# Performance work log

Hardware: AMD Instinct MI355X
Metric: run time of the kernel (lower is better)

Reference implementation:

```python
import jax, jax.numpy as jnp
import numpy as np

EPS_NORM = 1e-12
EPS_POS = 1e-05
MARGIN = 0.5


def l2_norm(x):
    # matches torch: x / sqrt(sum(x^2, axis=1) + 1e-12)
    norm = jnp.sqrt(jnp.sum(x * x, axis=1) + EPS_NORM)
    return x / norm[:, None]


def setup_inputs() -> dict:
    key = jax.random.key(0)
    k1, k2, k3, k4 = jax.random.split(key, 4)
    n, d, n_classes = 8192, 1024, 1024
    inputs_col = jax.random.normal(k1, (n, d), dtype=jnp.float32)
    inputs_row = jax.random.normal(k2, (n, d), dtype=jnp.float32)
    targets_col = jax.random.randint(k3, (n,), 0, n_classes)
    target_row = jax.random.randint(k4, (n,), 0, n_classes)
    return {"inputs_col": inputs_col, "targets_col": targets_col,
            "inputs_row": inputs_row, "target_row": target_row}


def reference(inputs_col, targets_col, inputs_row, target_row):
    n = inputs_col.shape[0]
    # [n, n] cosine similarity matrix
    sim = l2_norm(inputs_col) @ l2_norm(inputs_row).T
    same = targets_col[:, None] == target_row[None, :]  # [n, n] bool
    pos_mask = same & (sim < 1.0 - EPS_POS)
    neg_mask = (~same) & (sim > MARGIN)
    pos_loss = jnp.sum(jnp.where(pos_mask, 1.0 - sim, 0.0), axis=1)  # [n]
    neg_loss = jnp.sum(jnp.where(neg_mask, sim, 0.0), axis=1)        # [n]
    has_pos = jnp.any(pos_mask, axis=1)  # rows without valid positives are skipped
    row_loss = jnp.where(has_pos, pos_loss + neg_loss, 0.0)
    return jnp.sum(row_loss) / n
```

## Files before the change

kernel.cpp:

```cpp
#include <hip/hip_runtime.h>


constexpr int N = 8192;
constexpr int D = 1024;
constexpr int NT = D / 32;

typedef short bf16x8 __attribute__((ext_vector_type(8)));
typedef float f32x4 __attribute__((ext_vector_type(4)));

static __device__ inline unsigned short f2bf(float f) {
  unsigned int u = __float_as_uint(f);
  unsigned int r = (u + 0x7fffu + ((u >> 16) & 1u)) >> 16;
  return (unsigned short)r;
}

__global__ __launch_bounds__(256) void normalize_kernel(
    const float* __restrict__ in_col, const float* __restrict__ in_row,
    unsigned short* __restrict__ out_col, unsigned short* __restrict__ out_row,
    unsigned int* __restrict__ zeroBase) {
  if (blockIdx.x < 96) zeroBase[blockIdx.x * 256 + threadIdx.x] = 0u;

  int r = blockIdx.x * 4 + (threadIdx.x >> 6);
  int lane = threadIdx.x & 63;
  const float* in =
      (r < N) ? in_col + (size_t)r * D : in_row + (size_t)(r - N) * D;
  unsigned short* out =
      (r < N) ? out_col + (size_t)r * D : out_row + (size_t)(r - N) * D;
  float4 v[4];
  float s = 0.f;
#pragma unroll
  for (int c = 0; c < 4; c++) {
    v[c] = ((const float4*)in)[lane + c * 64];
    s += v[c].x * v[c].x + v[c].y * v[c].y + v[c].z * v[c].z + v[c].w * v[c].w;
  }
#pragma unroll
  for (int off = 32; off >= 1; off >>= 1) s += __shfl_xor(s, off, 64);
  float inv = 1.0f / sqrtf(s + 1e-12f);
#pragma unroll
  for (int c = 0; c < 4; c++) {
    ushort4 o;
    o.x = f2bf(v[c].x * inv);
    o.y = f2bf(v[c].y * inv);
    o.z = f2bf(v[c].z * inv);
    o.w = f2bf(v[c].w * inv);
    ((ushort4*)out)[lane + c * 64] = o;
  }
}

__global__ __launch_bounds__(256, 2) void loss_kernel(
    const unsigned short* __restrict__ An, const unsigned short* __restrict__ Bn,
    const int* __restrict__ tc, const int* __restrict__ tr,
    float* __restrict__ lossG, int* __restrict__ hasG) {
  __shared__ unsigned short lds[24576];
  char* ldsb = (char*)lds;
  const char* ldsc = (const char*)lds;

  const int tid = threadIdx.x;
  const int lane = tid & 63;
  const int wid = tid >> 6;
  const int wr = wid >> 1;
  const int wc = wid & 1;

  const int bid = blockIdx.x;
  const int xcd = bid & 7, s = bid >> 3;
  const int iBase = (s >> 3) * 256;
  const int jBase = (xcd * 8 + (s & 7)) * 128;

  const int frow = lane & 15;
  const int kx = ((lane >> 4) * 16) ^ ((lane & 6) << 3);
  int rowA[8], rowB[4];
#pragma unroll
  for (int m = 0; m < 8; m++) rowA[m] = (wr * 128 + m * 16 + frow) * 64;
#pragma unroll
  for (int n = 0; n < 4; n++) rowB[n] = 32768 + (wc * 64 + n * 16 + frow) * 64;

  const int srow = tid >> 2;
  const int c16 = tid & 3;
  const int kswz = (c16 ^ ((srow >> 1) & 3)) * 8;
  const unsigned short* aS[4];
  const unsigned short* bS[2];
#pragma unroll
  for (int p = 0; p < 4; p++)
    aS[p] = An + (size_t)(iBase + srow + 64 * p) * D + kswz;
#pragma unroll
  for (int p = 0; p < 2; p++)
    bS[p] = Bn + (size_t)(jBase + srow + 64 * p) * D + kswz;

#define GLDS(g, l)                                                        \
  __builtin_amdgcn_global_load_lds(                                       \
      (const __attribute__((address_space(1))) void*)(g),                 \
      (__attribute__((address_space(3))) void*)(l), 16, 0, 0)

#define STAGE(tt, P)                                                          \
  do {                                                                        \
    const int _ko = ((tt) & 31) * 32;                                         \
    _Pragma("unroll") for (int p = 0; p < 4; p++)                             \
        GLDS(aS[p] + _ko, ldsb + (P)*16384 + p * 4096 + wid * 1024);          \
    _Pragma("unroll") for (int p = 0; p < 2; p++)                             \
        GLDS(bS[p] + _ko, ldsb + 32768 + (P)*8192 + p * 4096 + wid * 1024);   \
  } while (0)

  f32x4 acc[8][4];
#pragma unroll
  for (int mi = 0; mi < 8; mi++)
#pragma unroll
    for (int ni = 0; ni < 4; ni++) acc[mi][ni] = (f32x4){0.f, 0.f, 0.f, 0.f};

  bf16x8 af[8], bf[4];

  STAGE(0, 0);
  __syncthreads();

#define TILE(T, P)                                                            \
  do {                                                                        \
    STAGE((T) + 1, 1 - (P));                                                  \
    _Pragma("unroll") for (int m = 0; m < 8; m++)                             \
        af[m] = *(const bf16x8*)(ldsc + (P)*16384 + rowA[m] + kx);            \
    _Pragma("unroll") for (int n = 0; n < 4; n++)                             \
        bf[n] = *(const bf16x8*)(ldsc + (P)*8192 + rowB[n] + kx);             \
    _Pragma("unroll") for (int m = 0; m < 8; m++)                             \
        _Pragma("unroll") for (int n = 0; n < 4; n++)                         \
            acc[m][n] = __builtin_amdgcn_mfma_f32_16x16x32_bf16(              \
                af[m], bf[n], acc[m][n], 0, 0, 0);                            \
    __syncthreads();                                                          \
  } while (0)

  for (int t2 = 0; t2 < NT / 2; ++t2) {
    const int t0 = 2 * t2;
    TILE(t0, 0);
    TILE(t0 + 1, 1);
  }
#undef TILE
#undef STAGE
#undef GLDS

  int trj[4];
#pragma unroll
  for (int ni = 0; ni < 4; ni++) trj[ni] = tr[jBase + wc * 64 + ni * 16 + frow];

#pragma unroll
  for (int mi = 0; mi < 8; mi++) {
#pragma unroll
    for (int r = 0; r < 4; r++) {
      const int i = iBase + wr * 128 + mi * 16 + (lane >> 4) * 4 + r;
      const int tci = tc[i];
      float v = 0.f;
      bool hasp = false;
#pragma unroll
      for (int ni = 0; ni < 4; ni++) {
        float s2 = acc[mi][ni][r];
        if (tci == trj[ni]) {
          if (s2 < 1.0f - 1e-5f) { v += 1.0f - s2; hasp = true; }
        } else if (s2 > 0.5f) {
          v += s2;
        }
      }
#pragma unroll
      for (int off = 1; off < 16; off <<= 1) v += __shfl_xor(v, off, 16);
      unsigned long long m = __ballot(hasp);
      bool rowHas = ((m >> ((lane >> 4) * 16)) & 0xFFFFull) != 0;
      if ((lane & 15) == 0) {
        if (v != 0.f) atomicAdd(&lossG[i], v);
        if (rowHas) atomicOr(&hasG[i], 1);
      }
    }
  }
}

__global__ __launch_bounds__(1024) void finalize_kernel(
    const float* __restrict__ lossG, const int* __restrict__ hasG,
    float* __restrict__ out) {
  int tid = threadIdx.x;
  float s = 0.f;
  for (int i = tid; i < N; i += 1024)
    if (hasG[i]) s += lossG[i];
#pragma unroll
  for (int off = 32; off >= 1; off >>= 1) s += __shfl_xor(s, off, 64);
  __shared__ float w16[16];
  if ((tid & 63) == 0) w16[tid >> 6] = s;
  __syncthreads();
  if (tid == 0) {
    float t = 0.f;
#pragma unroll
    for (int w = 0; w < 16; w++) t += w16[w];
    out[0] = t / (float)N;
  }
}

extern "C" void kernel_launch(void* const* d_in, const int* in_sizes, int n_in,
                              void* d_out, int out_size, void* d_ws, size_t ws_size,
                              hipStream_t stream) {
  const float* in_col = (const float*)d_in[0];
  const int* tcol = (const int*)d_in[1];
  const float* in_row = (const float*)d_in[2];
  const int* trow = (const int*)d_in[3];
  float* out = (float*)d_out;

  char* ws = (char*)d_ws;
  float* lossG = (float*)ws;
  int* hasG = (int*)(ws + (size_t)N * 4);
  unsigned short* colN = (unsigned short*)(ws + (size_t)N * 8);
  unsigned short* rowN = colN + (size_t)N * D;

  normalize_kernel<<<(2 * N) / 4, 256, 0, stream>>>(in_col, in_row, colN, rowN,
                                                    (unsigned int*)ws);
  loss_kernel<<<2048, 256, 0, stream>>>(colN, rowN, tcol, trow, lossG, hasG);
  finalize_kernel<<<1, 1024, 0, stream>>>(lossG, hasG, out);
}
```

Baseline: 288.7 us.

## Switch similarity GEMM to FP8 e4m3 with scaled MFMA 16x16x128

The normalize kernel now writes the L2-normalized rows as FP8 e4m3 instead of bf16. The loss kernel uses the MI355X scaled f8f6f4 MFMA with K=128 per instruction, on 128x128 output tiles and a 4096-block grid, with a reworked LDS swizzle. This halves the operand bytes and raises matrix throughput per instruction. The risk is accuracy: FP8 rounding of the similarities can flip threshold comparisons near 0.5 and 1-1e-5, which changes the loss value.

```diff
diff --git a/kernel.cpp b/kernel.cpp
--- a/kernel.cpp
+++ b/kernel.cpp
@@ -3,29 +3,40 @@
 
 constexpr int N = 8192;
 constexpr int D = 1024;
-constexpr int NT = D / 32;
-
-typedef short bf16x8 __attribute__((ext_vector_type(8)));
+
+typedef int i32x4 __attribute__((ext_vector_type(4)));
+typedef int i32x8 __attribute__((ext_vector_type(8)));
 typedef float f32x4 __attribute__((ext_vector_type(4)));
 
-static __device__ inline unsigned short f2bf(float f) {
-  unsigned int u = __float_as_uint(f);
-  unsigned int r = (u + 0x7fffu + ((u >> 16) & 1u)) >> 16;
-  return (unsigned short)r;
+static __device__ inline unsigned int f2fp8(float x) {
+  unsigned int u = __float_as_uint(x);
+  unsigned int sgn = (u >> 24) & 0x80u;
+  float a = __uint_as_float(u & 0x7fffffffu);
+  unsigned int bits;
+  if (a < 0.015625f) {
+    bits = (unsigned int)__float2int_rn(a * 512.0f);
+  } else {
+    unsigned int v = __float_as_uint(a);
+    unsigned int e = v >> 23;
+    unsigned int m = v & 0x7fffffu;
+    unsigned int mr = (m + 0x7ffffu + ((m >> 20) & 1u)) >> 20;
+    bits = ((e - 120u) << 3) + mr;
+  }
+  return sgn | bits;
 }
 
 __global__ __launch_bounds__(256) void normalize_kernel(
     const float* __restrict__ in_col, const float* __restrict__ in_row,
-    unsigned short* __restrict__ out_col, unsigned short* __restrict__ out_row,
+    unsigned int* __restrict__ out_col, unsigned int* __restrict__ out_row,
     unsigned int* __restrict__ zeroBase) {
-  if (blockIdx.x < 96) zeroBase[blockIdx.x * 256 + threadIdx.x] = 0u;
+  if (blockIdx.x < 64) zeroBase[blockIdx.x * 256 + threadIdx.x] = 0u;
 
   int r = blockIdx.x * 4 + (threadIdx.x >> 6);
   int lane = threadIdx.x & 63;
   const float* in =
       (r < N) ? in_col + (size_t)r * D : in_row + (size_t)(r - N) * D;
-  unsigned short* out =
-      (r < N) ? out_col + (size_t)r * D : out_row + (size_t)(r - N) * D;
+  unsigned int* out =
+      ((r < N) ? out_col : out_row) + (size_t)(r < N ? r : r - N) * (D / 4);
   float4 v[4];
   float s = 0.f;
 #pragma unroll
@@ -38,22 +49,17 @@
   float inv = 1.0f / sqrtf(s + 1e-12f);
 #pragma unroll
   for (int c = 0; c < 4; c++) {
-    ushort4 o;
-    o.x = f2bf(v[c].x * inv);
-    o.y = f2bf(v[c].y * inv);
-    o.z = f2bf(v[c].z * inv);
-    o.w = f2bf(v[c].w * inv);
-    ((ushort4*)out)[lane + c * 64] = o;
+    unsigned int u = f2fp8(v[c].x * inv) | (f2fp8(v[c].y * inv) << 8) |
+                     (f2fp8(v[c].z * inv) << 16) | (f2fp8(v[c].w * inv) << 24);
+    out[lane + c * 64] = u;
   }
 }
 
 __global__ __launch_bounds__(256, 2) void loss_kernel(
-    const unsigned short* __restrict__ An, const unsigned short* __restrict__ Bn,
+    const unsigned char* __restrict__ An, const unsigned char* __restrict__ Bn,
     const int* __restrict__ tc, const int* __restrict__ tr,
     float* __restrict__ lossG, int* __restrict__ hasG) {
-  __shared__ unsigned short lds[24576];
-  char* ldsb = (char*)lds;
-  const char* ldsc = (const char*)lds;
+  __shared__ char lds[65536];
 
   const int tid = threadIdx.x;
   const int lane = tid & 63;
@@ -63,93 +69,100 @@
 
   const int bid = blockIdx.x;
   const int xcd = bid & 7, s = bid >> 3;
-  const int iBase = (s >> 3) * 256;
+  const int iBase = (s >> 3) * 128;
   const int jBase = (xcd * 8 + (s & 7)) * 128;
 
   const int frow = lane & 15;
-  const int kx = ((lane >> 4) * 16) ^ ((lane & 6) << 3);
-  int rowA[8], rowB[4];
-#pragma unroll
-  for (int m = 0; m < 8; m++) rowA[m] = (wr * 128 + m * 16 + frow) * 64;
-#pragma unroll
-  for (int n = 0; n < 4; n++) rowB[n] = 32768 + (wc * 64 + n * 16 + frow) * 64;
-
-  const int srow = tid >> 2;
-  const int c16 = tid & 3;
-  const int kswz = (c16 ^ ((srow >> 1) & 3)) * 8;
-  const unsigned short* aS[4];
-  const unsigned short* bS[2];
-#pragma unroll
-  for (int p = 0; p < 4; p++)
-    aS[p] = An + (size_t)(iBase + srow + 64 * p) * D + kswz;
-#pragma unroll
-  for (int p = 0; p < 2; p++)
-    bS[p] = Bn + (size_t)(jBase + srow + 64 * p) * D + kswz;
+  const int cg = lane >> 4;
+  const int klo = ((2 * cg) ^ (frow & 7)) * 16;
+  const int khi = ((2 * cg + 1) ^ (frow & 7)) * 16;
+  int rowA[4], rowB[4];
+#pragma unroll
+  for (int f = 0; f < 4; f++) rowA[f] = (wr * 64 + f * 16 + frow) * 128;
+#pragma unroll
+  for (int f = 0; f < 4; f++)
+    rowB[f] = 32768 + (wc * 64 + f * 16 + frow) * 128;
+
+  const int srow = tid >> 3;
+  const int schunk = (tid & 7) ^ ((tid >> 3) & 7);
+  const unsigned char* aS[4];
+  const unsigned char* bS[4];
+#pragma unroll
+  for (int i = 0; i < 4; i++) {
+    aS[i] = An + (size_t)(iBase + i * 32 + srow) * D + schunk * 16;
+    bS[i] = Bn + (size_t)(jBase + i * 32 + srow) * D + schunk * 16;
+  }
 
 #define GLDS(g, l)                                                        \
   __builtin_amdgcn_global_load_lds(                                       \
       (const __attribute__((address_space(1))) void*)(g),                 \
       (__attribute__((address_space(3))) void*)(l), 16, 0, 0)
 
-#define STAGE(tt, P)                                                          \
-  do {                                                                        \
-    const int _ko = ((tt) & 31) * 32;                                         \
-    _Pragma("unroll") for (int p = 0; p < 4; p++)                             \
-        GLDS(aS[p] + _ko, ldsb + (P)*16384 + p * 4096 + wid * 1024);          \
-    _Pragma("unroll") for (int p = 0; p < 2; p++)                             \
-        GLDS(bS[p] + _ko, ldsb + 32768 + (P)*8192 + p * 4096 + wid * 1024);   \
+#define STAGE(st, P)                                                      \
+  do {                                                                    \
+    _Pragma("unroll") for (int i = 0; i < 4; i++)                         \
+        GLDS(aS[i] + (st) * 128, lds + (P)*16384 + i * 4096 + wid * 1024);\
+    _Pragma("unroll") for (int i = 0; i < 4; i++)                         \
+        GLDS(bS[i] + (st) * 128,                                          \
+             lds + 32768 + (P)*16384 + i * 4096 + wid * 1024);            \
   } while (0)
 
-  f32x4 acc[8][4];
-#pragma unroll
-  for (int mi = 0; mi < 8; mi++)
-#pragma unroll
-    for (int ni = 0; ni < 4; ni++) acc[mi][ni] = (f32x4){0.f, 0.f, 0.f, 0.f};
-
-  bf16x8 af[8], bf[4];
+  f32x4 acc[4][4];
+#pragma unroll
+  for (int a = 0; a < 4; a++)
+#pragma unroll
+    for (int b = 0; b < 4; b++) acc[a][b] = (f32x4){0.f, 0.f, 0.f, 0.f};
 
   STAGE(0, 0);
   __syncthreads();
 
-#define TILE(T, P)                                                            \
-  do {                                                                        \
-    STAGE((T) + 1, 1 - (P));                                                  \
-    _Pragma("unroll") for (int m = 0; m < 8; m++)                             \
-        af[m] = *(const bf16x8*)(ldsc + (P)*16384 + rowA[m] + kx);            \
-    _Pragma("unroll") for (int n = 0; n < 4; n++)                             \
-        bf[n] = *(const bf16x8*)(ldsc + (P)*8192 + rowB[n] + kx);             \
-    _Pragma("unroll") for (int m = 0; m < 8; m++)                             \
-        _Pragma("unroll") for (int n = 0; n < 4; n++)                         \
-            acc[m][n] = __builtin_amdgcn_mfma_f32_16x16x32_bf16(              \
-                af[m], bf[n], acc[m][n], 0, 0, 0);                            \
-    __syncthreads();                                                          \
-  } while (0)
-
-  for (int t2 = 0; t2 < NT / 2; ++t2) {
-    const int t0 = 2 * t2;
-    TILE(t0, 0);
-    TILE(t0 + 1, 1);
-  }
-#undef TILE
+#pragma unroll
+  for (int t = 0; t < 8; t++) {
+    const int P = t & 1;
+    if (t < 7) STAGE(t + 1, P ^ 1);
+    i32x8 af[4], bf[4];
+#pragma unroll
+    for (int f = 0; f < 4; f++) {
+      i32x4 lo = *(const i32x4*)(lds + P * 16384 + rowA[f] + klo);
+      i32x4 hi = *(const i32x4*)(lds + P * 16384 + rowA[f] + khi);
+      af[f][0] = lo[0]; af[f][1] = lo[1]; af[f][2] = lo[2]; af[f][3] = lo[3];
+      af[f][4] = hi[0]; af[f][5] = hi[1]; af[f][6] = hi[2]; af[f][7] = hi[3];
+    }
+#pragma unroll
+    for (int f = 0; f < 4; f++) {
+      i32x4 lo = *(const i32x4*)(lds + P * 16384 + rowB[f] + klo);
+      i32x4 hi = *(const i32x4*)(lds + P * 16384 + rowB[f] + khi);
+      bf[f][0] = lo[0]; bf[f][1] = lo[1]; bf[f][2] = lo[2]; bf[f][3] = lo[3];
+      bf[f][4] = hi[0]; bf[f][5] = hi[1]; bf[f][6] = hi[2]; bf[f][7] = hi[3];
+    }
+#pragma unroll
+    for (int a = 0; a < 4; a++)
+#pragma unroll
+      for (int b = 0; b < 4; b++)
+        acc[a][b] = __builtin_amdgcn_mfma_scale_f32_16x16x128_f8f6f4(
+            af[a], bf[b], acc[a][b], 0, 0,
+            0, 127, 0, 127);
+    __syncthreads();
+  }
 #undef STAGE
 #undef GLDS
 
   int trj[4];
 #pragma unroll
-  for (int ni = 0; ni < 4; ni++) trj[ni] = tr[jBase + wc * 64 + ni * 16 + frow];
-
-#pragma unroll
-  for (int mi = 0; mi < 8; mi++) {
+  for (int f = 0; f < 4; f++) trj[f] = tr[jBase + wc * 64 + f * 16 + frow];
+
+#pragma unroll
+  for (int a = 0; a < 4; a++) {
 #pragma unroll
     for (int r = 0; r < 4; r++) {
-      const int i = iBase + wr * 128 + mi * 16 + (lane >> 4) * 4 + r;
+      const int i = iBase + wr * 64 + a * 16 + (lane >> 4) * 4 + r;
       const int tci = tc[i];
       float v = 0.f;
       bool hasp = false;
 #pragma unroll
-      for (int ni = 0; ni < 4; ni++) {
-        float s2 = acc[mi][ni][r];
-        if (tci == trj[ni]) {
+      for (int b = 0; b < 4; b++) {
+        float s2 = acc[a][b][r];
+        if (tci == trj[b]) {
           if (s2 < 1.0f - 1e-5f) { v += 1.0f - s2; hasp = true; }
         } else if (s2 > 0.5f) {
           v += s2;
@@ -199,11 +212,12 @@
   char* ws = (char*)d_ws;
   float* lossG = (float*)ws;
   int* hasG = (int*)(ws + (size_t)N * 4);
-  unsigned short* colN = (unsigned short*)(ws + (size_t)N * 8);
-  unsigned short* rowN = colN + (size_t)N * D;
-
-  normalize_kernel<<<(2 * N) / 4, 256, 0, stream>>>(in_col, in_row, colN, rowN,
-                                                    (unsigned int*)ws);
-  loss_kernel<<<2048, 256, 0, stream>>>(colN, rowN, tcol, trow, lossG, hasG);
+  unsigned char* colN = (unsigned char*)(ws + (size_t)N * 8);
+  unsigned char* rowN = colN + (size_t)N * D;
+
+  normalize_kernel<<<(2 * N) / 4, 256, 0, stream>>>(
+      in_col, in_row, (unsigned int*)colN, (unsigned int*)rowN,
+      (unsigned int*)ws);
+  loss_kernel<<<4096, 256, 0, stream>>>(colN, rowN, tcol, trow, lossG, hasG);
   finalize_kernel<<<1, 1024, 0, stream>>>(lossG, hasG, out);
 }
```

Result: slower. 882.5 us (+205.7%).
